# Performance work log

Hardware: AMD Instinct MI355X
Metric: run time of the kernel (lower is better)

Reference implementation:

```python
import jax, jax.numpy as jnp
import numpy as np

N_HEADS, HEAD_OUT, IN_DIM = 4, 32, 128
HID = N_HEADS * HEAD_OUT  # 128, concat=True
N_NODES, N_EDGES, N_GRAPHS = 50000, 800000, 512
NEG_SLOPE = 0.2


def setup_inputs() -> dict:
    key = jax.random.key(0)
    ks = jax.random.split(key, 8)
    x = jax.random.normal(ks[0], (N_NODES, IN_DIM), jnp.float32)
    edge_index = jax.random.randint(ks[1], (2, N_EDGES), 0, N_NODES, dtype=jnp.int32)
    batch_index = jnp.sort(jax.random.randint(ks[2], (N_NODES,), 0, N_GRAPHS, dtype=jnp.int32))
    s_in = 1.0 / np.sqrt(IN_DIM)
    s_h = 1.0 / np.sqrt(HID)
    W_l = jax.random.normal(ks[3], (IN_DIM, HID), jnp.float32) * s_in   # GATv2 lin_l (source)
    W_r = jax.random.normal(ks[4], (IN_DIM, HID), jnp.float32) * s_in   # GATv2 lin_r (target)
    att = jax.random.normal(ks[5], (N_HEADS, HEAD_OUT), jnp.float32) * (1.0 / np.sqrt(HEAD_OUT))
    bias = jnp.zeros((HID,), jnp.float32)                                # GATv2 output bias
    W_rel = jax.random.normal(ks[6], (HID, 1), jnp.float32) * s_h        # SAGPool GraphConv lin_rel
    b_rel = jnp.zeros((1,), jnp.float32)
    W_root = jax.random.normal(ks[7], (HID, 1), jnp.float32) * s_h       # SAGPool GraphConv lin_root (no bias)
    return dict(x=x, edge_index=edge_index, batch_index=batch_index,
                W_l=W_l, W_r=W_r, att=att, bias=bias,
                W_rel=W_rel, b_rel=b_rel, W_root=W_root)


def _segment_softmax(logits, seg, num_segments):
    m = jax.ops.segment_max(logits, seg, num_segments=num_segments)
    m = jnp.where(jnp.isfinite(m), m, 0.0)
    e = jnp.exp(logits - m[seg])
    d = jax.ops.segment_sum(e, seg, num_segments=num_segments)
    return e / jnp.maximum(d[seg], 1e-16)


def _forward(x, edge_index, batch_index, W_l, W_r, att, bias, W_rel, b_rel, W_root):
    N = x.shape[0]
    src0, dst0 = edge_index[0], edge_index[1]
    # --- GATv2Conv (add_self_loops=True default) ---
    loop = jnp.arange(N, dtype=src0.dtype)
    src = jnp.concatenate([src0, loop])
    dst = jnp.concatenate([dst0, loop])
    xl = (x @ W_l).reshape(N, N_HEADS, HEAD_OUT)  # source transform
    xr = (x @ W_r).reshape(N, N_HEADS, HEAD_OUT)  # target transform
    e = jax.nn.leaky_relu(xl[src] + xr[dst], NEG_SLOPE)          # [E+N, H, C]
    logits = jnp.einsum('ehc,hc->eh', e, att)                     # [E+N, H]
    alpha = _segment_softmax(logits, dst, N)                      # neighborhood softmax per dst
    out = jax.ops.segment_sum(xl[src] * alpha[:, :, None], dst, num_segments=N)
    out = out.reshape(N, HID) + bias                              # concat heads + bias
    # --- SAGPooling(min_score=-1): GraphConv score -> per-graph softmax; all nodes kept ---
    agg = jax.ops.segment_sum(out[src0], dst0, num_segments=N)    # add-aggregate neighbors
    score = (agg @ W_rel + b_rel + out @ W_root).squeeze(-1)      # [N]
    s = _segment_softmax(score, batch_index, N_GRAPHS)            # softmax over each graph
    att_x = out * s[:, None]
    # --- global_add_pool ---
    g = jax.ops.segment_sum(att_x, batch_index, num_segments=N_GRAPHS)  # [B, HID]
    return out, g


def reference(x, edge_index, batch_index, W_l, W_r, att, bias, W_rel, b_rel, W_root):
    return _forward(x, edge_index, batch_index, W_l, W_r, att, bias, W_rel, b_rel, W_root)
```

## Files before the change

### kernel.cpp

```cpp
#include <hip/hip_runtime.h>
#include <cfloat>

#define N_NODES 50000
#define E0      800000
#define EP      850000
#define NGRAPH  512
#define HID     128
#define NB_SCAN 49
#define NEG_SLOPE 0.2f

__global__ __launch_bounds__(256) void k_hist(const int* __restrict__ dst0, int* __restrict__ cnt){
  int e = blockIdx.x*256 + threadIdx.x;
  if (e < E0) atomicAdd(&cnt[dst0[e]], 1);
}

__global__ __launch_bounds__(256) void k_scan1(const int* __restrict__ cnt, int* __restrict__ bsum){
  __shared__ int red[256];
  int tid = threadIdx.x;
  int base = blockIdx.x*1024 + tid*4;
  int s = 0;
  #pragma unroll
  for (int i=0;i<4;++i){ int idx = base+i; if (idx < N_NODES) s += cnt[idx] + 1; }
  red[tid] = s; __syncthreads();
  for (int off=128; off>0; off>>=1){ if (tid<off) red[tid]+=red[tid+off]; __syncthreads(); }
  if (tid==0) bsum[blockIdx.x] = red[0];
}

__global__ void k_scan2(const int* __restrict__ bsum, int* __restrict__ boff, int* __restrict__ row_start){
  if (threadIdx.x == 0){
    int run = 0;
    for (int b=0;b<NB_SCAN;++b){ boff[b] = run; run += bsum[b]; }
    row_start[N_NODES] = run;
  }
}

__global__ __launch_bounds__(256) void k_scan3(const int* __restrict__ cnt, const int* __restrict__ boff,
    int* __restrict__ row_start, int* __restrict__ fill){
  __shared__ int sbuf[256];
  int tid = threadIdx.x;
  int base = blockIdx.x*1024 + tid*4;
  int v[4]; int ts = 0;
  #pragma unroll
  for (int i=0;i<4;++i){ int idx=base+i; v[i] = (idx<N_NODES)? cnt[idx]+1 : 0; ts += v[i]; }
  sbuf[tid] = ts; __syncthreads();
  for (int off=1; off<256; off<<=1){
    int add = (tid>=off)? sbuf[tid-off] : 0;
    __syncthreads();
    sbuf[tid] += add;
    __syncthreads();
  }
  int run = boff[blockIdx.x] + sbuf[tid] - ts;
  #pragma unroll
  for (int i=0;i<4;++i){
    int idx = base+i;
    if (idx < N_NODES){ row_start[idx]=run; fill[idx]=run; run += v[i]; }
  }
}

__global__ __launch_bounds__(256) void k_scatter(const int* __restrict__ src0, const int* __restrict__ dst0,
    int* __restrict__ fill, int* __restrict__ col_src){
  int i = blockIdx.x*256 + threadIdx.x;
  if (i >= EP) return;
  int s, d;
  if (i < E0){ s = src0[i]; d = dst0[i]; }
  else       { s = i - E0;  d = s; }
  int slot = atomicAdd(&fill[d], 1);
  col_src[slot] = s;
}

__global__ __launch_bounds__(256) void k_gemm(const float* __restrict__ x,
    const float* __restrict__ Wl, const float* __restrict__ Wr,
    float* __restrict__ xl, float* __restrict__ xr){
  __shared__ float xs[64][128];
  __shared__ float wbuf[8][256];
  int tid = threadIdx.x;
  int n0 = blockIdx.x * 64;
  #pragma unroll
  for (int it=0; it<8; ++it){
    int f = it*1024 + tid*4;
    int r = f >> 7, c = f & 127;
    float4 v = make_float4(0.f,0.f,0.f,0.f);
    if (n0 + r < N_NODES) v = *(const float4*)&x[(size_t)(n0+r)*128 + c];
    *(float4*)&xs[r][c] = v;
  }
  int cgrp = tid & 31, ngrp = tid >> 5;
  float acc[8][8];
  #pragma unroll
  for (int i=0;i<8;++i)
    #pragma unroll
    for (int j=0;j<8;++j) acc[i][j]=0.f;

  for (int kc=0; kc<16; ++kc){
    #pragma unroll
    for (int it=0; it<2; ++it){
      int f = it*1024 + tid*4;
      int kk = f >> 8, c = f & 255;
      int k = kc*8 + kk;
      float4 wv = (c < 128) ? *(const float4*)&Wl[k*128 + c]
                            : *(const float4*)&Wr[k*128 + (c-128)];
      *(float4*)&wbuf[kk][c] = wv;
    }
    __syncthreads();
    #pragma unroll
    for (int kk=0; kk<8; ++kk){
      int k = kc*8 + kk;
      float a[8], bv[8];
      #pragma unroll
      for (int i=0;i<8;++i) a[i] = xs[ngrp*8+i][k];
      #pragma unroll
      for (int j=0;j<8;++j) bv[j] = wbuf[kk][cgrp + 32*j];
      #pragma unroll
      for (int i=0;i<8;++i)
        #pragma unroll
        for (int j=0;j<8;++j) acc[i][j] = fmaf(a[i], bv[j], acc[i][j]);
    }
    __syncthreads();
  }
  #pragma unroll
  for (int i=0;i<8;++i){
    int node = n0 + ngrp*8 + i;
    if (node < N_NODES){
      #pragma unroll
      for (int j=0;j<4;++j){
        xl[(size_t)node*128 + cgrp + 32*j] = acc[i][j];
        xr[(size_t)node*128 + cgrp + 32*j] = acc[i][j+4];
      }
    }
  }
}

__device__ __forceinline__ float lrdot(float2 v, float2 xr2, float2 at2){
  float ex = v.x + xr2.x, ey = v.y + xr2.y;
  ex = ex > 0.f ? ex : NEG_SLOPE*ex;
  ey = ey > 0.f ? ey : NEG_SLOPE*ey;
  return ex*at2.x + ey*at2.y;
}

__global__ __launch_bounds__(256) void k_attn(
    const float* __restrict__ xl, const float* __restrict__ xr,
    const int* __restrict__ row_start, const int* __restrict__ col_src,
    const float* __restrict__ attv, const float* __restrict__ bias,
    const float* __restrict__ Wrel, const float* __restrict__ Wroot,
    const float* __restrict__ brel,
    float* __restrict__ out, float* __restrict__ pbuf, float* __restrict__ score){
  int wid = blockIdx.x*4 + (threadIdx.x >> 6);
  if (wid >= N_NODES) return;
  int lane = threadIdx.x & 63;
  int c2 = lane*2;
  float2 xr2 = *(const float2*)&xr[(size_t)wid*128 + c2];
  float2 at2 = *(const float2*)&attv[c2];
  int row = row_start[wid];
  int deg = row_start[wid+1] - row;
  float d = 0.f, ax = 0.f, ay = 0.f;
  int i = 0;
  for (; i+4 <= deg; i += 4){
    int s0 = col_src[row+i+0];
    int s1 = col_src[row+i+1];
    int s2 = col_src[row+i+2];
    int s3 = col_src[row+i+3];
    float2 v0 = *(const float2*)&xl[(size_t)s0*128 + c2];
    float2 v1 = *(const float2*)&xl[(size_t)s1*128 + c2];
    float2 v2 = *(const float2*)&xl[(size_t)s2*128 + c2];
    float2 v3 = *(const float2*)&xl[(size_t)s3*128 + c2];
    float t0 = lrdot(v0, xr2, at2);
    float t1 = lrdot(v1, xr2, at2);
    float t2 = lrdot(v2, xr2, at2);
    float t3 = lrdot(v3, xr2, at2);
    t0 += __shfl_xor(t0,1); t1 += __shfl_xor(t1,1); t2 += __shfl_xor(t2,1); t3 += __shfl_xor(t3,1);
    t0 += __shfl_xor(t0,2); t1 += __shfl_xor(t1,2); t2 += __shfl_xor(t2,2); t3 += __shfl_xor(t3,2);
    t0 += __shfl_xor(t0,4); t1 += __shfl_xor(t1,4); t2 += __shfl_xor(t2,4); t3 += __shfl_xor(t3,4);
    t0 += __shfl_xor(t0,8); t1 += __shfl_xor(t1,8); t2 += __shfl_xor(t2,8); t3 += __shfl_xor(t3,8);
    float w0 = __expf(t0), w1 = __expf(t1), w2 = __expf(t2), w3 = __expf(t3);
    d += (w0 + w1) + (w2 + w3);
    ax = fmaf(w3, v3.x, fmaf(w2, v2.x, fmaf(w1, v1.x, fmaf(w0, v0.x, ax))));
    ay = fmaf(w3, v3.y, fmaf(w2, v2.y, fmaf(w1, v1.y, fmaf(w0, v0.y, ay))));
  }
  for (; i < deg; ++i){
    int s = col_src[row+i];
    float2 v = *(const float2*)&xl[(size_t)s*128 + c2];
    float t = lrdot(v, xr2, at2);
    t += __shfl_xor(t,1); t += __shfl_xor(t,2); t += __shfl_xor(t,4); t += __shfl_xor(t,8);
    float w = __expf(t);
    d += w;
    ax = fmaf(w, v.x, ax);
    ay = fmaf(w, v.y, ay);
  }
  float inv = 1.f/d;
  float ox = fmaf(ax, inv, bias[c2]);
  float oy = fmaf(ay, inv, bias[c2+1]);
  *(float2*)&out[(size_t)wid*128 + c2] = make_float2(ox, oy);
  float pv = ox*Wrel[c2]  + oy*Wrel[c2+1];
  float rv = ox*Wroot[c2] + oy*Wroot[c2+1];
  #pragma unroll
  for (int off=1; off<64; off<<=1){
    pv += __shfl_xor(pv, off);
    rv += __shfl_xor(rv, off);
  }
  if (lane == 0){
    pbuf[wid]  = pv;
    score[wid] = brel[0] + rv;
  }
}

__global__ __launch_bounds__(256) void k_score(
    const int* __restrict__ row_start, const int* __restrict__ col_src,
    const float* __restrict__ pbuf, float* __restrict__ score){
  int n = blockIdx.x*256 + threadIdx.x;
  if (n >= N_NODES) return;
  int row = row_start[n], deg = row_start[n+1]-row;
  float sc = score[n] - pbuf[n];
  for (int i=0;i<deg;++i) sc += pbuf[col_src[row+i]];
  score[n] = sc;
}

__device__ __forceinline__ int lbound(const int* __restrict__ a, int n, int v){
  int lo=0, hi=n;
  while (lo < hi){ int mid=(lo+hi)>>1; if (a[mid] < v) lo = mid+1; else hi = mid; }
  return lo;
}

__global__ __launch_bounds__(128) void k_pool(
    const int* __restrict__ batch, const float* __restrict__ score,
    const float* __restrict__ out, float* __restrict__ g){
  int b = blockIdx.x;
  int tid = threadIdx.x;
  int start = lbound(batch, N_NODES, b);
  int end   = lbound(batch, N_NODES, b+1);
  __shared__ float red[128];
  __shared__ float sl[128];
  float lm = -FLT_MAX;
  for (int i=start+tid; i<end; i+=128) lm = fmaxf(lm, score[i]);
  red[tid]=lm; __syncthreads();
  for (int off=64; off>0; off>>=1){ if (tid<off) red[tid]=fmaxf(red[tid],red[tid+off]); __syncthreads(); }
  float m = red[0]; __syncthreads();
  float ls = 0.f;
  for (int i=start+tid; i<end; i+=128) ls += __expf(score[i]-m);
  red[tid]=ls; __syncthreads();
  for (int off=64; off>0; off>>=1){ if (tid<off) red[tid]+=red[tid+off]; __syncthreads(); }
  float inv = 1.f / fmaxf(red[0], 1e-16f);
  __syncthreads();
  float acc = 0.f;
  for (int base=start; base<end; base+=128){
    int idx = base+tid;
    sl[tid] = (idx<end) ? __expf(score[idx]-m)*inv : 0.f;
    __syncthreads();
    int lim = min(128, end-base);
    for (int jj=0; jj<lim; ++jj) acc = fmaf(out[(size_t)(base+jj)*128 + tid], sl[jj], acc);
    __syncthreads();
  }
  g[b*128 + tid] = acc;
}

extern "C" void kernel_launch(void* const* d_in, const int* in_sizes, int n_in,
                              void* d_out, int out_size, void* d_ws, size_t ws_size,
                              hipStream_t stream){
  const float* x    = (const float*)d_in[0];
  const int*   ei   = (const int*)d_in[1];
  const int*   batch= (const int*)d_in[2];
  const float* Wl   = (const float*)d_in[3];
  const float* Wr   = (const float*)d_in[4];
  const float* attv = (const float*)d_in[5];
  const float* bias = (const float*)d_in[6];
  const float* Wrel = (const float*)d_in[7];
  const float* brel = (const float*)d_in[8];
  const float* Wroot= (const float*)d_in[9];
  const int* src0 = ei;
  const int* dst0 = ei + E0;

  float* out = (float*)d_out;
  float* g   = out + (size_t)N_NODES*HID;

  float* xl = (float*)d_ws;
  float* xr = xl + (size_t)N_NODES*HID;
  int* cnt       = (int*)(xr + (size_t)N_NODES*HID);
  int* row_start = cnt + N_NODES;
  int* fill      = row_start + N_NODES + 1;
  int* bsum      = fill + N_NODES;
  int* boff      = bsum + NB_SCAN;
  int* col_src   = boff + NB_SCAN;
  float* pbuf    = (float*)(col_src + EP);
  float* score   = pbuf + N_NODES;

  hipMemsetAsync(cnt, 0, N_NODES*sizeof(int), stream);
  k_gemm   <<<dim3((N_NODES+63)/64), 256, 0, stream>>>(x, Wl, Wr, xl, xr);
  k_hist   <<<dim3((E0+255)/256),    256, 0, stream>>>(dst0, cnt);
  k_scan1  <<<dim3(NB_SCAN),         256, 0, stream>>>(cnt, bsum);
  k_scan2  <<<dim3(1),                64, 0, stream>>>(bsum, boff, row_start);
  k_scan3  <<<dim3(NB_SCAN),         256, 0, stream>>>(cnt, boff, row_start, fill);
  k_scatter<<<dim3((EP+255)/256),    256, 0, stream>>>(src0, dst0, fill, col_src);
  k_attn   <<<dim3(N_NODES/4),       256, 0, stream>>>(xl, xr, row_start, col_src,
                                                       attv, bias, Wrel, Wroot, brel,
                                                       out, pbuf, score);
  k_score  <<<dim3((N_NODES+255)/256),256, 0, stream>>>(row_start, col_src, pbuf, score);
  k_pool   <<<dim3(NGRAPH),          128, 0, stream>>>(batch, score, out, g);
}
```

Before: 342.6 us.

## Restructure projection GEMM with smaller node tiles and direct vectorized weight loads

Rewrites the node-feature projection kernel to use 32-node tiles with 128 threads. Weights are now read straight from global memory as float4 instead of being staged through shared memory, and each thread accumulates 4 contiguous columns of both xl and xr so results go out as float4 stores. This drops the per-chunk weight staging and its barriers, coalesces the output writes and launches more blocks. The trade-off is that weight reuse now relies on the cache rather than shared memory, and each block does less work.

Result: no change. 337.2 us (-1.6%).

```diff
diff --git a/kernel.cpp b/kernel.cpp
--- a/kernel.cpp
+++ b/kernel.cpp
@@ -8,6 +8,7 @@
 #define HID     128
 #define NB_SCAN 49
 #define NEG_SLOPE 0.2f
+#define GTILE   32
 
 __global__ __launch_bounds__(256) void k_hist(const int* __restrict__ dst0, int* __restrict__ cnt){
   int e = blockIdx.x*256 + threadIdx.x;
@@ -68,63 +69,63 @@
   col_src[slot] = s;
 }
 
-__global__ __launch_bounds__(256) void k_gemm(const float* __restrict__ x,
+__global__ __launch_bounds__(128) void k_gemm(const float* __restrict__ x,
     const float* __restrict__ Wl, const float* __restrict__ Wr,
     float* __restrict__ xl, float* __restrict__ xr){
-  __shared__ float xs[64][128];
-  __shared__ float wbuf[8][256];
-  int tid = threadIdx.x;
-  int n0 = blockIdx.x * 64;
+  __shared__ float xs[GTILE][128];
+  int tid = threadIdx.x;
+  int n0 = blockIdx.x * GTILE;
   #pragma unroll
   for (int it=0; it<8; ++it){
-    int f = it*1024 + tid*4;
+    int f = it*512 + tid*4;
     int r = f >> 7, c = f & 127;
     float4 v = make_float4(0.f,0.f,0.f,0.f);
     if (n0 + r < N_NODES) v = *(const float4*)&x[(size_t)(n0+r)*128 + c];
     *(float4*)&xs[r][c] = v;
   }
+  __syncthreads();
   int cgrp = tid & 31, ngrp = tid >> 5;
-  float acc[8][8];
+  int c4 = cgrp*4;
+  float accl[8][4], accr[8][4];
   #pragma unroll
   for (int i=0;i<8;++i)
     #pragma unroll
-    for (int j=0;j<8;++j) acc[i][j]=0.f;
-
-  for (int kc=0; kc<16; ++kc){
-    #pragma unroll
-    for (int it=0; it<2; ++it){
-      int f = it*1024 + tid*4;
-      int kk = f >> 8, c = f & 255;
-      int k = kc*8 + kk;
-      float4 wv = (c < 128) ? *(const float4*)&Wl[k*128 + c]
-                            : *(const float4*)&Wr[k*128 + (c-128)];
-      *(float4*)&wbuf[kk][c] = wv;
+    for (int j=0;j<4;++j){ accl[i][j]=0.f; accr[i][j]=0.f; }
+
+  for (int k=0; k<128; k+=4){
+    float4 a4[8];
+    #pragma unroll
+    for (int i=0;i<8;++i) a4[i] = *(const float4*)&xs[ngrp*8+i][k];
+    float4 wl4[4], wr4[4];
+    #pragma unroll
+    for (int kk=0;kk<4;++kk){
+      wl4[kk] = *(const float4*)&Wl[(size_t)(k+kk)*128 + c4];
+      wr4[kk] = *(const float4*)&Wr[(size_t)(k+kk)*128 + c4];
     }
-    __syncthreads();
-    #pragma unroll
-    for (int kk=0; kk<8; ++kk){
-      int k = kc*8 + kk;
-      float a[8], bv[8];
+    #pragma unroll
+    for (int i=0;i<8;++i){
+      const float* av = (const float*)&a4[i];
       #pragma unroll
-      for (int i=0;i<8;++i) a[i] = xs[ngrp*8+i][k];
-      #pragma unroll
-      for (int j=0;j<8;++j) bv[j] = wbuf[kk][cgrp + 32*j];
-      #pragma unroll
-      for (int i=0;i<8;++i)
+      for (int kk=0;kk<4;++kk){
+        float a = av[kk];
+        const float* wl = (const float*)&wl4[kk];
+        const float* wr = (const float*)&wr4[kk];
         #pragma unroll
-        for (int j=0;j<8;++j) acc[i][j] = fmaf(a[i], bv[j], acc[i][j]);
+        for (int j=0;j<4;++j){
+          accl[i][j] = fmaf(a, wl[j], accl[i][j]);
+          accr[i][j] = fmaf(a, wr[j], accr[i][j]);
+        }
+      }
     }
-    __syncthreads();
   }
   #pragma unroll
   for (int i=0;i<8;++i){
     int node = n0 + ngrp*8 + i;
     if (node < N_NODES){
-      #pragma unroll
-      for (int j=0;j<4;++j){
-        xl[(size_t)node*128 + cgrp + 32*j] = acc[i][j];
-        xr[(size_t)node*128 + cgrp + 32*j] = acc[i][j+4];
-      }
+      float4 vl = make_float4(accl[i][0], accl[i][1], accl[i][2], accl[i][3]);
+      float4 vr = make_float4(accr[i][0], accr[i][1], accr[i][2], accr[i][3]);
+      *(float4*)&xl[(size_t)node*128 + c4] = vl;
+      *(float4*)&xr[(size_t)node*128 + c4] = vr;
     }
   }
 }
@@ -282,7 +283,7 @@
   float* score   = pbuf + N_NODES;
 
   hipMemsetAsync(cnt, 0, N_NODES*sizeof(int), stream);
-  k_gemm   <<<dim3((N_NODES+63)/64), 256, 0, stream>>>(x, Wl, Wr, xl, xr);
+  k_gemm   <<<dim3((N_NODES+GTILE-1)/GTILE), 128, 0, stream>>>(x, Wl, Wr, xl, xr);
   k_hist   <<<dim3((E0+255)/256),    256, 0, stream>>>(dst0, cnt);
   k_scan1  <<<dim3(NB_SCAN),         256, 0, stream>>>(cnt, bsum);
   k_scan2  <<<dim3(1),                64, 0, stream>>>(bsum, boff, row_start);
```
